# Performance work log

Measured on AMD Instinct MI355X. Metric: run time of the kernel, lower is better.

The kernel has to match this reference:

```python
import jax, jax.numpy as jnp
import numpy as np

# Reversible solver constants (init kwargs / solve args)
L = 0.999          # coupling parameter l
H = 1.0 / 64.0     # step size h
T_END = 1.0        # terminal time T
N_STEPS = int(T_END / H)  # 64 sequential steps

B, D, HID = 4096, 512, 2048


def setup_inputs() -> dict:
    key = jax.random.key(0)
    k0, k1, k2, k3 = jax.random.split(key, 4)
    s1 = 1.0 / np.sqrt(D).astype(np.float32)
    s2 = 1.0 / np.sqrt(HID).astype(np.float32)
    return {
        "y0": jax.random.normal(k0, (B, D), jnp.float32),
        "W1": jax.random.normal(k1, (D, HID), jnp.float32) * s1,
        "b1": jnp.zeros((HID,), jnp.float32),
        "wt": jax.random.normal(k2, (HID,), jnp.float32) * 0.1,
        "W2": jax.random.normal(k3, (HID, D), jnp.float32) * s2,
        "b2": jnp.zeros((D,), jnp.float32),
    }


def reference(y0, W1, b1, wt, W2, b2):
    # MLP vector field vf(t, y): [B, D] -> [B, D]
    def vf(t, y):
        hidden = jnp.tanh(y @ W1 + b1 + t * wt)  # [B, HID]
        return hidden @ W2 + b2                   # [B, D]

    # Explicit Euler solver step: step(vf, h, t, y) = h * vf(t, y)
    def euler_step(hh, t, y):
        return hh * vf(t, y)

    # Reversible forward step (faithful to _solve_forward.forward_step)
    def forward_step(carry, _):
        t0, y0_, z0 = carry
        t1 = t0 + H
        y1 = L * y0_ + (1.0 - L) * z0 + euler_step(H, t0, z0)
        z1 = z0 - euler_step(-H, t1, y1)
        return (t1, y1, z1), None

    t0 = jnp.zeros((), jnp.float32)
    (tN, yN, zN), _ = jax.lax.scan(forward_step, (t0, y0, y0), None, length=N_STEPS)
    return yN
```

## Files before the change

kernel.cpp:

```cpp
#include <hip/hip_runtime.h>
#include <hip/hip_bf16.h>

typedef __bf16 bf16x8 __attribute__((ext_vector_type(8)));
typedef float f32x4 __attribute__((ext_vector_type(4)));
typedef unsigned short u16;

#define GLD_LDS16(gp, lp) __builtin_amdgcn_global_load_lds( \
    (const __attribute__((address_space(1))) unsigned int*)(gp), \
    (__attribute__((address_space(3))) unsigned int*)(lp), 16, 0, 0)

__device__ __forceinline__ float tanh_fast(float x) {
  float e = __expf(2.0f * x);
  return 1.0f - __fdividef(2.0f, e + 1.0f);
}

__device__ __forceinline__ u16 bf16_rn(float x) {
  union { float f; unsigned u; } v; v.f = x;
  unsigned r = v.u + 0x7fffu + ((v.u >> 16) & 1u);
  return (u16)(r >> 16);
}

template <int BM, int BN, int BK, int K, int MODE, int NTL>
__global__ __launch_bounds__(256)
void gemm_fused(const u16* __restrict__ A, const u16* __restrict__ Bt,
                const float* __restrict__ bias, const float* __restrict__ wt,
                float tval,
                const float* __restrict__ y_in, const float* __restrict__ z_in,
                float* __restrict__ out32, u16* __restrict__ out_bf, int N) {
  constexpr int NS = BK / 64;
  constexpr int WTM = BM / 2, WTN = BN / 2;
  constexpr int FM = WTM / 16, FN = WTN / 16;
  constexpr int ACH = BM * BK * 2 / 1024;
  constexpr int BCH = BN * BK * 2 / 1024;
  constexpr int CPS_A = BM / 8;
  constexpr int CPS_B = BN / 8;
  constexpr int MT = 4096 / BM;
  constexpr int MPX = MT / 8;

  __shared__ u16 As[NS * BM * 64];
  __shared__ u16 Bs[NS * BN * 64];

  const int tid = threadIdx.x;
  const int wave = tid >> 6;
  const int lane = tid & 63;
  const int wm = wave >> 1, wn = wave & 1;
  const int l15 = lane & 15, kg = lane >> 4;

  const int wg = blockIdx.x;
  const int xcd = wg & 7;
  const int j = wg >> 3;
  const int bm0 = (xcd * MPX + j / NTL) * BM;
  const int bn0 = (j % NTL) * BN;

  f32x4 acc[FM][FN];
#pragma unroll
  for (int m = 0; m < FM; ++m)
#pragma unroll
    for (int n = 0; n < FN; ++n) acc[m][n] = (f32x4){0.f, 0.f, 0.f, 0.f};

  const int sr = lane >> 3;
  const int sc = (lane & 7) * 8;

  const u16* Ag = A + (size_t)bm0 * K;
  const u16* Bg = Bt + (size_t)bn0 * K;

  for (int kt = 0; kt < K / BK; ++kt) {
    const u16* Ak = Ag + kt * BK;
    const u16* Bk = Bg + kt * BK;
#pragma unroll
    for (int i = 0; i < ACH / 4; ++i) {
      const int ch = wave + i * 4;
      const int kh = ch / CPS_A;
      const int rg = ch % CPS_A;
      GLD_LDS16(Ak + (size_t)(rg * 8 + sr) * K + kh * 64 + sc,
                (char*)As + ch * 1024);
    }
#pragma unroll
    for (int i = 0; i < BCH / 4; ++i) {
      const int ch = wave + i * 4;
      const int kh = ch / CPS_B;
      const int rg = ch % CPS_B;
      GLD_LDS16(Bk + (size_t)(rg * 8 + sr) * K + kh * 64 + sc,
                (char*)Bs + ch * 1024);
    }
    __syncthreads();
#pragma unroll
    for (int ks = 0; ks < 2 * NS; ++ks) {
      const int kh = ks >> 1;
      const int kc = (ks & 1) * 32 + kg * 8;
      bf16x8 af[FM], bfr[FN];
#pragma unroll
      for (int m = 0; m < FM; ++m)
        af[m] = *reinterpret_cast<const bf16x8*>(
            &As[(kh * BM + wm * WTM + m * 16 + l15) * 64 + kc]);
#pragma unroll
      for (int n = 0; n < FN; ++n)
        bfr[n] = *reinterpret_cast<const bf16x8*>(
            &Bs[(kh * BN + wn * WTN + n * 16 + l15) * 64 + kc]);
#pragma unroll
      for (int m = 0; m < FM; ++m)
#pragma unroll
        for (int n = 0; n < FN; ++n)
          acc[m][n] =
              __builtin_amdgcn_mfma_f32_16x16x32_bf16(af[m], bfr[n], acc[m][n], 0, 0, 0);
    }
    __syncthreads();
  }

#pragma unroll
  for (int n = 0; n < FN; ++n) {
    const int col = bn0 + wn * WTN + n * 16 + l15;
    const float bv = bias[col];
    const float wv = (MODE == 0) ? wt[col] : 0.f;
#pragma unroll
    for (int m = 0; m < FM; ++m) {
      const int row0 = bm0 + wm * WTM + m * 16 + kg * 4;
#pragma unroll
      for (int r = 0; r < 4; ++r) {
        const size_t idx = (size_t)(row0 + r) * N + col;
        const float a = acc[m][n][r];
        if (MODE == 0) {
          const float x = a + bv + tval * wv;
          out_bf[idx] = bf16_rn(tanh_fast(x));
        } else if (MODE == 1) {
          const float v = 0.999f * y_in[idx] + 0.001f * z_in[idx] +
                          0.015625f * (a + bv);
          out32[idx] = v;
          out_bf[idx] = bf16_rn(v);
        } else {
          const float v = z_in[idx] + 0.015625f * (a + bv);
          out32[idx] = v;
          out_bf[idx] = bf16_rn(v);
        }
      }
    }
  }
}

__global__ void transpose_bf16(const float* __restrict__ in, u16* __restrict__ out,
                               int R, int C) {
  __shared__ float tile[32][33];
  const int bx = blockIdx.x * 32;
  const int by = blockIdx.y * 32;
  const int tx = threadIdx.x, ty = threadIdx.y;
#pragma unroll
  for (int i = 0; i < 32; i += 8)
    tile[ty + i][tx] = in[(size_t)(by + ty + i) * C + (bx + tx)];
  __syncthreads();
#pragma unroll
  for (int i = 0; i < 32; i += 8)
    out[(size_t)(bx + ty + i) * R + (by + tx)] = bf16_rn(tile[tx][ty + i]);
}

__global__ void init_state(const float* __restrict__ y0, float* __restrict__ y32,
                           float* __restrict__ z32, u16* __restrict__ zbf, int n) {
  const int i = blockIdx.x * blockDim.x + threadIdx.x;
  if (i < n) {
    const float v = y0[i];
    y32[i] = v;
    z32[i] = v;
    zbf[i] = bf16_rn(v);
  }
}

extern "C" void kernel_launch(void* const* d_in, const int* in_sizes, int n_in,
                              void* d_out, int out_size, void* d_ws, size_t ws_size,
                              hipStream_t stream) {
  const float* y0 = (const float*)d_in[0];
  const float* W1 = (const float*)d_in[1];
  const float* b1 = (const float*)d_in[2];
  const float* wt = (const float*)d_in[3];
  const float* W2 = (const float*)d_in[4];
  const float* b2 = (const float*)d_in[5];

  constexpr int B = 4096, D = 512, HID = 2048, NSTEP = 64;
  constexpr float Hh = 1.0f / 64.0f;

  char* ws = (char*)d_ws;
  u16* W1t = (u16*)ws; ws += (size_t)HID * D * 2;
  u16* W2t = (u16*)ws; ws += (size_t)D * HID * 2;
  u16* hid = (u16*)ws; ws += (size_t)B * HID * 2;
  float* z32 = (float*)ws; ws += (size_t)B * D * 4;
  u16* ybf = (u16*)ws; ws += (size_t)B * D * 2;
  u16* zbf = (u16*)ws; ws += (size_t)B * D * 2;
  float* y32 = (float*)d_out;

  transpose_bf16<<<dim3(HID / 32, D / 32), dim3(32, 8), 0, stream>>>(W1, W1t, D, HID);
  transpose_bf16<<<dim3(D / 32, HID / 32), dim3(32, 8), 0, stream>>>(W2, W2t, HID, D);
  init_state<<<(B * D + 255) / 256, 256, 0, stream>>>(y0, y32, z32, zbf, B * D);

  for (int s = 0; s < NSTEP; ++s) {
    const float t0 = (float)s * Hh;
    const float t1 = (float)(s + 1) * Hh;
    gemm_fused<128, 128, 128, 512, 0, 16><<<512, 256, 0, stream>>>(
        zbf, W1t, b1, wt, t0, nullptr, nullptr, nullptr, hid, HID);
    gemm_fused<64, 64, 256, 2048, 1, 8><<<512, 256, 0, stream>>>(
        hid, W2t, b2, nullptr, 0.f, y32, z32, y32, ybf, D);
    gemm_fused<128, 128, 128, 512, 0, 16><<<512, 256, 0, stream>>>(
        ybf, W1t, b1, wt, t1, nullptr, nullptr, nullptr, hid, HID);
    gemm_fused<64, 64, 256, 2048, 2, 8><<<512, 256, 0, stream>>>(
        hid, W2t, b2, nullptr, 0.f, nullptr, z32, z32, zbf, D);
  }
}
```

Measured before the change: 5.161 ms.

## Double-buffer LDS tiles with async global-to-LDS prefetch pipeline

Splits shared memory into two slabs and issues global_load_lds for tile t+2 while computing on tile t. Explicit vmcnt waits and raw s_barriers replace the earlier load-sync-compute-sync loop. BK is halved so the doubled buffers keep the same LDS footprint and every wave issues exactly 8 loads per tile. This aims to hide global memory latency behind MFMA work, at the cost of more K iterations and more barriers.

```diff
diff --git a/kernel.cpp b/kernel.cpp
--- a/kernel.cpp
+++ b/kernel.cpp
@@ -36,9 +36,14 @@
   constexpr int CPS_B = BN / 8;
   constexpr int MT = 4096 / BM;
   constexpr int MPX = MT / 8;
-
-  __shared__ u16 As[NS * BM * 64];
-  __shared__ u16 Bs[NS * BN * 64];
+  constexpr int NT = K / BK;
+  constexpr int SLAB_A = NS * BM * 64;
+  constexpr int SLAB_B = NS * BN * 64;
+  static_assert(ACH / 4 + BCH / 4 == 8, "vmcnt(8) schedule needs 8 loads/wave");
+  static_assert(NT >= 2, "pipeline needs >=2 K-tiles");
+
+  __shared__ u16 As[2][SLAB_A];
+  __shared__ u16 Bs[2][SLAB_B];
 
   const int tid = threadIdx.x;
   const int wave = tid >> 6;
@@ -64,26 +69,40 @@
   const u16* Ag = A + (size_t)bm0 * K;
   const u16* Bg = Bt + (size_t)bn0 * K;
 
-  for (int kt = 0; kt < K / BK; ++kt) {
-    const u16* Ak = Ag + kt * BK;
-    const u16* Bk = Bg + kt * BK;
+  auto issue = [&](int t) {
+    const u16* Ak = Ag + (size_t)t * BK;
+    const u16* Bk = Bg + (size_t)t * BK;
+    char* ab = (char*)As[t & 1];
+    char* bb = (char*)Bs[t & 1];
 #pragma unroll
     for (int i = 0; i < ACH / 4; ++i) {
       const int ch = wave + i * 4;
       const int kh = ch / CPS_A;
       const int rg = ch % CPS_A;
-      GLD_LDS16(Ak + (size_t)(rg * 8 + sr) * K + kh * 64 + sc,
-                (char*)As + ch * 1024);
+      GLD_LDS16(Ak + (size_t)(rg * 8 + sr) * K + kh * 64 + sc, ab + ch * 1024);
     }
 #pragma unroll
     for (int i = 0; i < BCH / 4; ++i) {
       const int ch = wave + i * 4;
       const int kh = ch / CPS_B;
       const int rg = ch % CPS_B;
-      GLD_LDS16(Bk + (size_t)(rg * 8 + sr) * K + kh * 64 + sc,
-                (char*)Bs + ch * 1024);
-    }
-    __syncthreads();
+      GLD_LDS16(Bk + (size_t)(rg * 8 + sr) * K + kh * 64 + sc, bb + ch * 1024);
+    }
+  };
+
+  issue(0);
+  issue(1);
+
+  for (int t = 0; t < NT; ++t) {
+    if (t + 1 < NT)
+      asm volatile("s_waitcnt vmcnt(8)" ::: "memory");
+    else
+      asm volatile("s_waitcnt vmcnt(0)" ::: "memory");
+    __builtin_amdgcn_sched_barrier(0);
+    __builtin_amdgcn_s_barrier();
+
+    const u16* Asl = As[t & 1];
+    const u16* Bsl = Bs[t & 1];
 #pragma unroll
     for (int ks = 0; ks < 2 * NS; ++ks) {
       const int kh = ks >> 1;
@@ -92,11 +111,11 @@
 #pragma unroll
       for (int m = 0; m < FM; ++m)
         af[m] = *reinterpret_cast<const bf16x8*>(
-            &As[(kh * BM + wm * WTM + m * 16 + l15) * 64 + kc]);
+            &Asl[(kh * BM + wm * WTM + m * 16 + l15) * 64 + kc]);
 #pragma unroll
       for (int n = 0; n < FN; ++n)
         bfr[n] = *reinterpret_cast<const bf16x8*>(
-            &Bs[(kh * BN + wn * WTN + n * 16 + l15) * 64 + kc]);
+            &Bsl[(kh * BN + wn * WTN + n * 16 + l15) * 64 + kc]);
 #pragma unroll
       for (int m = 0; m < FM; ++m)
 #pragma unroll
@@ -104,7 +123,9 @@
           acc[m][n] =
               __builtin_amdgcn_mfma_f32_16x16x32_bf16(af[m], bfr[n], acc[m][n], 0, 0, 0);
     }
-    __syncthreads();
+    __builtin_amdgcn_sched_barrier(0);
+    __builtin_amdgcn_s_barrier();
+    if (t + 2 < NT) issue(t + 2);
   }
 
 #pragma unroll
@@ -192,13 +213,13 @@
   for (int s = 0; s < NSTEP; ++s) {
     const float t0 = (float)s * Hh;
     const float t1 = (float)(s + 1) * Hh;
-    gemm_fused<128, 128, 128, 512, 0, 16><<<512, 256, 0, stream>>>(
+    gemm_fused<128, 128, 64, 512, 0, 16><<<512, 256, 0, stream>>>(
         zbf, W1t, b1, wt, t0, nullptr, nullptr, nullptr, hid, HID);
-    gemm_fused<64, 64, 256, 2048, 1, 8><<<512, 256, 0, stream>>>(
+    gemm_fused<64, 64, 128, 2048, 1, 8><<<512, 256, 0, stream>>>(
         hid, W2t, b2, nullptr, 0.f, y32, z32, y32, ybf, D);
-    gemm_fused<128, 128, 128, 512, 0, 16><<<512, 256, 0, stream>>>(
+    gemm_fused<128, 128, 64, 512, 0, 16><<<512, 256, 0, stream>>>(
         ybf, W1t, b1, wt, t1, nullptr, nullptr, nullptr, hid, HID);
-    gemm_fused<64, 64, 256, 2048, 2, 8><<<512, 256, 0, stream>>>(
+    gemm_fused<64, 64, 128, 2048, 2, 8><<<512, 256, 0, stream>>>(
         hid, W2t, b2, nullptr, 0.f, nullptr, z32, z32, zbf, D);
   }
 }
```

New measurement: 5.402 ms. 4.7% more time.
